# Kernel tuning notes

Hardware: AMD Instinct MI355X
Metric: run time of the kernel (lower is better)

## Reference

```python
import jax, jax.numpy as jnp
import numpy as np

DIM = 512
BATCH, SEQ = 4, 4096


def setup_inputs() -> dict:
    key = jax.random.key(0)
    kx, kq, kk, kv, ko = jax.random.split(key, 5)
    s = DIM ** -0.5  # fan-in style init scale for stability
    return {
        "x": jax.random.normal(kx, (BATCH, SEQ, DIM), dtype=jnp.float32),
        "Wq": jax.random.normal(kq, (DIM, DIM), dtype=jnp.float32) * s,
        "Wk": jax.random.normal(kk, (DIM, DIM), dtype=jnp.float32) * s,
        "Wv": jax.random.normal(kv, (DIM, DIM), dtype=jnp.float32) * s,
        "Wo": jax.random.normal(ko, (DIM, DIM), dtype=jnp.float32) * s,
    }


def reference(x, Wq, Wk, Wv, Wo):
    # x: [B, S, D]; projections (torch Linear, no bias -> x @ W here)
    q = jnp.einsum('bsd,dk->bsk', x, Wq)  # [B,S,K]
    k = jnp.einsum('bsd,dk->bsk', x, Wk)  # [B,S,K]
    v = jnp.einsum('bsd,dv->bsv', x, Wv)  # [B,S,V]

    # sequential recurrence: M_t = M_{t-1} + v_t k_t^T ; y_t = M_t q_t
    def step(M, qkv_t):
        q_t, k_t, v_t = qkv_t  # each [B, K] / [B, V]
        M = M + v_t[:, :, None] * k_t[:, None, :]  # [B, V, K]
        y_t = jnp.einsum('bvk,bk->bv', M, q_t)
        return M, y_t

    M0 = jnp.zeros((x.shape[0], Wv.shape[1], Wk.shape[1]), dtype=x.dtype)
    qT = jnp.swapaxes(q, 0, 1)  # [S,B,K]
    kT = jnp.swapaxes(k, 0, 1)
    vT = jnp.swapaxes(v, 0, 1)
    _, ys = jax.lax.scan(step, M0, (qT, kT, vT))  # ys: [S,B,V]
    y = jnp.swapaxes(ys, 0, 1)  # [B,S,V]
    return jnp.einsum('bsv,vd->bsd', y, Wo)
```

## Files before the change

kernel.cpp:

```cpp
#include <hip/hip_runtime.h>
#include <hip/hip_bf16.h>

typedef __attribute__((ext_vector_type(8))) short bf16x8;
typedef __attribute__((ext_vector_type(4))) float f32x4;

__device__ inline short f2bf(float f) {
    __hip_bfloat16 h = __float2bfloat16(f);
    short s;
    __builtin_memcpy(&s, &h, 2);
    return s;
}
__device__ inline float bf2f(short s) {
    unsigned int u = ((unsigned int)(unsigned short)s) << 16;
    float f;
    __builtin_memcpy(&f, &u, 4);
    return f;
}

__device__ inline void cp16_async(const void* g, void* l) {
    __builtin_amdgcn_global_load_lds(
        (const __attribute__((address_space(1))) void*)g,
        (__attribute__((address_space(3))) void*)l, 16, 0, 0);
}


__global__ void prep_kernel(const float* __restrict__ x, short* __restrict__ Xb,
                            const float* __restrict__ W0, const float* __restrict__ W1,
                            const float* __restrict__ W2, const float* __restrict__ W3,
                            short* __restrict__ W4T) {
    int bid = blockIdx.x;
    if (bid < 8192) {
        int i = bid * 256 + threadIdx.x;
        float4 f = ((const float4*)x)[i];
        union { short s[4]; int2 v; } u;
        u.s[0] = f2bf(f.x); u.s[1] = f2bf(f.y); u.s[2] = f2bf(f.z); u.s[3] = f2bf(f.w);
        ((int2*)Xb)[i] = u.v;
    } else {
        int i = (bid - 8192) * 256 + threadIdx.x;
        int w = i >> 18;
        int r = i & 262143;
        int n = r >> 9, k = r & 511;
        const float* W = (w == 0) ? W0 : (w == 1) ? W1 : (w == 2) ? W2 : W3;
        W4T[i] = f2bf(W[k * 512 + n]);
    }
}


#define LDS_DECL __shared__ short sA0[4096], sA1[4096], sB0[4096], sB1[4096]

__device__ inline void mfma_kloop64(const short* __restrict__ A, int lda,
                                    const short* __restrict__ B, int ldb,
                                    int Kd, f32x4* acc,
                                    short* sA0, short* sA1, short* sB0, short* sB1) {
    const int tid = threadIdx.x, lane = tid & 63, wv = tid >> 6;
    const int quad = lane >> 4, lr = lane & 15;
    const int wr = (wv >> 1) * 64, wc = (wv & 1) * 64;
    const int c0 = tid, c1 = tid + 256;
    const int r0 = c0 >> 2, k80 = (c0 & 3) * 8;
    const int r1 = c1 >> 2, k81 = (c1 & 3) * 8;

    for (int k0 = 0; k0 < Kd; k0 += 64) {
        __syncthreads();
        cp16_async(A + (size_t)r0 * lda + k0 + k80,      sA0 + c0 * 8);
        cp16_async(A + (size_t)r1 * lda + k0 + k81,      sA0 + c1 * 8);
        cp16_async(A + (size_t)r0 * lda + k0 + 32 + k80, sA1 + c0 * 8);
        cp16_async(A + (size_t)r1 * lda + k0 + 32 + k81, sA1 + c1 * 8);
        cp16_async(B + (size_t)r0 * ldb + k0 + k80,      sB0 + c0 * 8);
        cp16_async(B + (size_t)r1 * ldb + k0 + k81,      sB0 + c1 * 8);
        cp16_async(B + (size_t)r0 * ldb + k0 + 32 + k80, sB1 + c0 * 8);
        cp16_async(B + (size_t)r1 * ldb + k0 + 32 + k81, sB1 + c1 * 8);
        __syncthreads();
#pragma unroll
        for (int half = 0; half < 2; ++half) {
            const short* pa = half ? sA1 : sA0;
            const short* pb = half ? sB1 : sB0;
            bf16x8 af[4], bfr[4];
#pragma unroll
            for (int i = 0; i < 4; ++i)
                af[i] = *(const bf16x8*)&pa[(wr + i * 16 + lr) * 32 + quad * 8];
#pragma unroll
            for (int j = 0; j < 4; ++j)
                bfr[j] = *(const bf16x8*)&pb[(wc + j * 16 + lr) * 32 + quad * 8];
#pragma unroll
            for (int i = 0; i < 4; ++i)
#pragma unroll
                for (int j = 0; j < 4; ++j)
                    acc[i * 4 + j] = __builtin_amdgcn_mfma_f32_16x16x32_bf16(af[i], bfr[j], acc[i * 4 + j], 0, 0, 0);
        }
    }
}

__device__ inline void store_out(float* p, float v) { *p = v; }
__device__ inline void store_out(short* p, float v) { *p = f2bf(v); }

template <typename OutT>
__device__ inline void store_tile128(OutT* C, int ldc, const f32x4* acc) {
    const int lane = threadIdx.x & 63, wv = threadIdx.x >> 6;
    const int quad = lane >> 4, lr = lane & 15;
    const int wr = (wv >> 1) * 64, wc = (wv & 1) * 64;
#pragma unroll
    for (int i = 0; i < 4; ++i)
#pragma unroll
        for (int j = 0; j < 4; ++j)
#pragma unroll
            for (int r = 0; r < 4; ++r)
                store_out(&C[(size_t)(wr + i * 16 + quad * 4 + r) * ldc + wc + j * 16 + lr],
                          acc[i * 4 + j][r]);
}

__global__ __launch_bounds__(256, 4) void proj_all(const short* __restrict__ Xb,
                                                   const short* __restrict__ W4T,
                                                   short* __restrict__ Qb, short* __restrict__ Kb,
                                                   short* __restrict__ Vt, short* __restrict__ Kt) {
    LDS_DECL;
    f32x4 acc[16];
#pragma unroll
    for (int i = 0; i < 16; ++i) acc[i] = (f32x4){0.f, 0.f, 0.f, 0.f};
    const int bid = blockIdx.x;
    const int lane = threadIdx.x & 63, wv = threadIdx.x >> 6;
    const int quad = lane >> 4, lr = lane & 15;
    const int wr = (wv >> 1) * 64, wc = (wv & 1) * 64;
    if (bid < 1024) {
        const int mt = bid >> 3, by = bid & 7;
        const short* At = Xb + (size_t)mt * 128 * 512;
        const short* Bt = W4T + (size_t)by * 128 * 512;
        short* Ct = ((by < 4) ? Qb : Kb) + (size_t)mt * 128 * 512 + (by & 3) * 128;
        mfma_kloop64(At, 512, Bt, 512, 512, acc, sA0, sA1, sB0, sB1);
        store_tile128(Ct, 512, acc);
        if (by >= 4) {
            const int b = mt >> 5;
            const int t0b = (mt & 31) * 128;
            const int f0 = (by - 4) * 128;
#pragma unroll
            for (int i = 0; i < 4; ++i)
#pragma unroll
                for (int j = 0; j < 4; ++j) {
                    int f = f0 + wc + j * 16 + lr;
                    int tt0 = t0b + wr + i * 16 + quad * 4;
                    short tmp[4];
#pragma unroll
                    for (int r = 0; r < 4; ++r) tmp[r] = f2bf(acc[i * 4 + j][r]);
                    *(int2*)&Kt[((size_t)b * 512 + f) * 4096 + tt0] = *(const int2*)tmp;
                }
        }
    } else {
        const int r = bid - 1024;
        const int b = r & 3, tt = (r >> 2) & 31, ft = r >> 7;
        const short* At = W4T + (size_t)2 * 262144 + (size_t)ft * 128 * 512;
        const short* Bt = Xb + ((size_t)b * 4096 + tt * 128) * 512;
        short* Ct = Vt + (size_t)b * 512 * 4096 + (size_t)ft * 128 * 4096 + tt * 128;
        mfma_kloop64(At, 512, Bt, 512, 512, acc, sA0, sA1, sB0, sB1);
        store_tile128(Ct, 4096, acc);
    }
}


__global__ __launch_bounds__(256, 4) void phaseA(const short* __restrict__ Vt,
                                                 const short* __restrict__ Kt,
                                                 short* __restrict__ AM) {
    LDS_DECL;
    const int bc = blockIdx.z, b = bc >> 4, c = bc & 15;
    const short* Ap = Vt + ((size_t)b * 512 + blockIdx.x * 128) * 4096 + c * 256;
    const short* Bp = Kt + ((size_t)b * 512 + blockIdx.y * 128) * 4096 + c * 256;
    short* Cp = AM + (size_t)bc * 262144 + (size_t)blockIdx.x * 128 * 512 + blockIdx.y * 128;
    f32x4 acc[16];
#pragma unroll
    for (int i = 0; i < 16; ++i) acc[i] = (f32x4){0.f, 0.f, 0.f, 0.f};
    mfma_kloop64(Ap, 4096, Bp, 4096, 256, acc, sA0, sA1, sB0, sB1);
    store_tile128(Cp, 512, acc);
}

__global__ __launch_bounds__(256, 4) void scan_phaseS(short* __restrict__ AM,
                                                      const short* __restrict__ Q,
                                                      const short* __restrict__ K,
                                                      short* __restrict__ P) {
    LDS_DECL;
    if (blockIdx.x < 512) {
        int i = blockIdx.x * 256 + threadIdx.x;
        int b = i >> 15;
        int vk8 = i & 32767;
        size_t base = (size_t)b * 16 * 262144 + (size_t)vk8 * 8;
        float acc[8];
#pragma unroll
        for (int s = 0; s < 8; ++s) acc[s] = 0.f;
        for (int c = 0; c < 16; ++c) {
            short* p = AM + base + (size_t)c * 262144;
            short in8[8];
            *(int4*)in8 = *(const int4*)p;
            short out8[8];
#pragma unroll
            for (int s = 0; s < 8; ++s) out8[s] = f2bf(acc[s]);
            *(int4*)p = *(const int4*)out8;
#pragma unroll
            for (int s = 0; s < 8; ++s) acc[s] += bf2f(in8[s]);
        }
        return;
    }
    const int e = blockIdx.x - 512;
    const int bc = e >> 2, mt = e & 1, nt = (e >> 1) & 1;
    if (mt < nt) return;
    const int b = bc >> 4, c = bc & 15;
    short* Pt = P + (size_t)bc * 65536 + (size_t)mt * 128 * 256 + nt * 128;
    const short* Ap = Q + ((size_t)(b * 4096 + c * 256 + mt * 128)) * 512;
    const short* Bp = K + ((size_t)(b * 4096 + c * 256 + nt * 128)) * 512;
    f32x4 acc[16];
#pragma unroll
    for (int i = 0; i < 16; ++i) acc[i] = (f32x4){0.f, 0.f, 0.f, 0.f};
    mfma_kloop64(Ap, 512, Bp, 512, 512, acc, sA0, sA1, sB0, sB1);
    const int lane = threadIdx.x & 63, wv = threadIdx.x >> 6;
    const int quad = lane >> 4, lr = lane & 15;
    const int wr = (wv >> 1) * 64, wc = (wv & 1) * 64;
    const bool diag = (mt == nt);
#pragma unroll
    for (int i = 0; i < 4; ++i)
#pragma unroll
        for (int j = 0; j < 4; ++j)
#pragma unroll
            for (int r = 0; r < 4; ++r) {
                int t = wr + i * 16 + quad * 4 + r;
                int jj = wc + j * 16 + lr;
                float v = (!diag || jj <= t) ? acc[i * 4 + j][r] : 0.f;
                Pt[(size_t)t * 256 + jj] = f2bf(v);
            }
}

__global__ __launch_bounds__(256, 4) void phaseY(const short* __restrict__ Q,
                                                 const short* __restrict__ Mpre,
                                                 const short* __restrict__ P,
                                                 const short* __restrict__ Vt,
                                                 short* __restrict__ Y) {
    LDS_DECL;
    const int bc = blockIdx.z, b = bc >> 4, c = bc & 15;
    const int mt = blockIdx.x, nt = blockIdx.y;
    f32x4 acc[16];
#pragma unroll
    for (int i = 0; i < 16; ++i) acc[i] = (f32x4){0.f, 0.f, 0.f, 0.f};
    const short* Ai = Q + ((size_t)(b * 4096 + c * 256 + mt * 128)) * 512;
    const short* Bi = Mpre + (size_t)bc * 262144 + (size_t)nt * 128 * 512;
    mfma_kloop64(Ai, 512, Bi, 512, 512, acc, sA0, sA1, sB0, sB1);
    const short* Ap = P + (size_t)bc * 65536 + (size_t)mt * 128 * 256;
    const short* Bv = Vt + ((size_t)b * 512 + nt * 128) * 4096 + c * 256;
    mfma_kloop64(Ap, 256, Bv, 4096, (mt + 1) * 128, acc, sA0, sA1, sB0, sB1);
    short* Cp = Y + ((size_t)(b * 4096 + c * 256 + mt * 128)) * 512 + nt * 128;
    store_tile128(Cp, 512, acc);
}

template <typename OutT>
__global__ __launch_bounds__(256, 4) void gemm128(const short* __restrict__ A, int lda,
                                                  const short* __restrict__ B, int ldb,
                                                  OutT* __restrict__ C, int ldc, int Kd) {
    LDS_DECL;
    const short* At = A + (size_t)blockIdx.x * 128 * lda;
    const short* Bt = B + (size_t)blockIdx.y * 128 * ldb;
    OutT* Ct = C + (size_t)blockIdx.x * 128 * ldc + blockIdx.y * 128;
    f32x4 acc[16];
#pragma unroll
    for (int i = 0; i < 16; ++i) acc[i] = (f32x4){0.f, 0.f, 0.f, 0.f};
    mfma_kloop64(At, lda, Bt, ldb, Kd, acc, sA0, sA1, sB0, sB1);
    store_tile128(Ct, ldc, acc);
}


extern "C" void kernel_launch(void* const* d_in, const int* in_sizes, int n_in,
                              void* d_out, int out_size, void* d_ws, size_t ws_size,
                              hipStream_t stream) {
    const float* x  = (const float*)d_in[0];
    const float* Wq = (const float*)d_in[1];
    const float* Wk = (const float*)d_in[2];
    const float* Wv = (const float*)d_in[3];
    const float* Wo = (const float*)d_in[4];
    float* out = (float*)d_out;

    const size_t NTD = 16384 * 512;

    short* ws  = (short*)d_ws;
    short* Xb  = ws;
    short* Qb  = Xb + NTD;
    short* Kb  = Qb + NTD;
    short* Kt  = Kb + NTD;
    short* Vt  = Kt + NTD;
    short* P   = Vt + NTD;
    short* W4T = P + 4194304;
    short* AM  = W4T + 1048576;
    short* Yb  = Kb;

    short* WoT = W4T + 3 * 262144;

    prep_kernel<<<12288, 256, 0, stream>>>(x, Xb, Wq, Wk, Wv, Wo, W4T);
    proj_all<<<1536, 256, 0, stream>>>(Xb, W4T, Qb, Kb, Vt, Kt);
    phaseA<<<dim3(4, 4, 64), 256, 0, stream>>>(Vt, Kt, AM);
    scan_phaseS<<<768, 256, 0, stream>>>(AM, Qb, Kb, P);
    phaseY<<<dim3(2, 4, 64), 256, 0, stream>>>(Qb, AM, P, Vt, Yb);
    gemm128<float><<<dim3(128, 4), 256, 0, stream>>>(Yb, 512, WoT, 512, out, 512, 512);
}
```

Baseline: 222.0 us.

## Widen projection and chunk-state GEMM tiles, transpose weights via LDS, flatten grids

Weight transposition in the prep kernel now stages 64x64 tiles through shared memory, so global reads and writes are coalesced instead of strided. The projection and chunk-state (phaseA) GEMMs move to 128x256 tiles with 32 accumulators per thread, which increases operand reuse and halves block counts. All kernels use 1D grids with launch bounds lowered to 2 waves-per-SIMD occupancy, and the output projection becomes a dedicated kernel. The wider tiles double LDS and register use, so fewer blocks fit per CU and latency hiding may suffer.

Measured after the change: 222.1 us. About the same (+0.0%).

```diff
diff --git a/kernel.cpp b/kernel.cpp
--- a/kernel.cpp
+++ b/kernel.cpp
@@ -23,30 +23,44 @@
         (__attribute__((address_space(3))) void*)l, 16, 0, 0);
 }
 
-
 __global__ void prep_kernel(const float* __restrict__ x, short* __restrict__ Xb,
                             const float* __restrict__ W0, const float* __restrict__ W1,
                             const float* __restrict__ W2, const float* __restrict__ W3,
                             short* __restrict__ W4T) {
-    int bid = blockIdx.x;
+    __shared__ short sT[64][72];
+    const int bid = blockIdx.x, tid = threadIdx.x;
     if (bid < 8192) {
-        int i = bid * 256 + threadIdx.x;
+        int i = bid * 256 + tid;
         float4 f = ((const float4*)x)[i];
         union { short s[4]; int2 v; } u;
         u.s[0] = f2bf(f.x); u.s[1] = f2bf(f.y); u.s[2] = f2bf(f.z); u.s[3] = f2bf(f.w);
         ((int2*)Xb)[i] = u.v;
-    } else {
-        int i = (bid - 8192) * 256 + threadIdx.x;
-        int w = i >> 18;
-        int r = i & 262143;
-        int n = r >> 9, k = r & 511;
-        const float* W = (w == 0) ? W0 : (w == 1) ? W1 : (w == 2) ? W2 : W3;
-        W4T[i] = f2bf(W[k * 512 + n]);
-    }
-}
-
-
-#define LDS_DECL __shared__ short sA0[4096], sA1[4096], sB0[4096], sB1[4096]
+        return;
+    }
+    const int wb = bid - 8192;
+    const int w = wb >> 6, r = wb & 63;
+    const int n0 = (r >> 3) * 64, k0 = (r & 7) * 64;
+    const float* W = (w == 0) ? W0 : (w == 1) ? W1 : (w == 2) ? W2 : W3;
+#pragma unroll
+    for (int rr = 0; rr < 4; ++rr) {
+        int c = rr * 256 + tid;
+        int row = c >> 4, col4 = (c & 15) * 4;
+        float4 f = *(const float4*)&W[(size_t)(k0 + row) * 512 + n0 + col4];
+        sT[col4 + 0][row] = f2bf(f.x);
+        sT[col4 + 1][row] = f2bf(f.y);
+        sT[col4 + 2][row] = f2bf(f.z);
+        sT[col4 + 3][row] = f2bf(f.w);
+    }
+    __syncthreads();
+#pragma unroll
+    for (int rr = 0; rr < 2; ++rr) {
+        int c = rr * 256 + tid;
+        int f = c >> 3, k8 = (c & 7) * 8;
+        int4 v = *(const int4*)&sT[f][k8];
+        *(int4*)&W4T[(size_t)w * 262144 + (size_t)(n0 + f) * 512 + k0 + k8] = v;
+    }
+}
+
 
 __device__ inline void mfma_kloop64(const short* __restrict__ A, int lda,
                                     const short* __restrict__ B, int ldb,
@@ -108,75 +122,142 @@
                           acc[i * 4 + j][r]);
 }
 
-__global__ __launch_bounds__(256, 4) void proj_all(const short* __restrict__ Xb,
-                                                   const short* __restrict__ W4T,
-                                                   short* __restrict__ Qb, short* __restrict__ Kb,
-                                                   short* __restrict__ Vt, short* __restrict__ Kt) {
-    LDS_DECL;
-    f32x4 acc[16];
-#pragma unroll
-    for (int i = 0; i < 16; ++i) acc[i] = (f32x4){0.f, 0.f, 0.f, 0.f};
-    const int bid = blockIdx.x;
+
+__device__ inline void mfma_kloop64_wide(const short* __restrict__ A, int lda,
+                                         const short* __restrict__ B, int ldb,
+                                         int Kd, f32x4* acc,
+                                         short* sA0, short* sA1, short* sB0, short* sB1) {
+    const int tid = threadIdx.x, lane = tid & 63, wv = tid >> 6;
+    const int quad = lane >> 4, lr = lane & 15;
+    const int wr = (wv >> 1) * 64, wc = (wv & 1) * 128;
+
+    for (int k0 = 0; k0 < Kd; k0 += 64) {
+        __syncthreads();
+#pragma unroll
+        for (int rr = 0; rr < 2; ++rr) {
+            int c = rr * 256 + tid;
+            int row = c >> 2, k8 = (c & 3) * 8;
+            cp16_async(A + (size_t)row * lda + k0 + k8,      sA0 + c * 8);
+            cp16_async(A + (size_t)row * lda + k0 + 32 + k8, sA1 + c * 8);
+        }
+#pragma unroll
+        for (int rr = 0; rr < 4; ++rr) {
+            int c = rr * 256 + tid;
+            int row = c >> 2, k8 = (c & 3) * 8;
+            cp16_async(B + (size_t)row * ldb + k0 + k8,      sB0 + c * 8);
+            cp16_async(B + (size_t)row * ldb + k0 + 32 + k8, sB1 + c * 8);
+        }
+        __syncthreads();
+#pragma unroll
+        for (int half = 0; half < 2; ++half) {
+            const short* pa = half ? sA1 : sA0;
+            const short* pb = half ? sB1 : sB0;
+            bf16x8 af[4], bfr[8];
+#pragma unroll
+            for (int i = 0; i < 4; ++i)
+                af[i] = *(const bf16x8*)&pa[(wr + i * 16 + lr) * 32 + quad * 8];
+#pragma unroll
+            for (int j = 0; j < 8; ++j)
+                bfr[j] = *(const bf16x8*)&pb[(wc + j * 16 + lr) * 32 + quad * 8];
+#pragma unroll
+            for (int i = 0; i < 4; ++i)
+#pragma unroll
+                for (int j = 0; j < 8; ++j)
+                    acc[i * 8 + j] = __builtin_amdgcn_mfma_f32_16x16x32_bf16(af[i], bfr[j], acc[i * 8 + j], 0, 0, 0);
+        }
+    }
+}
+
+template <typename OutT>
+__device__ inline void store_tile_wide(OutT* C, int ldc, const f32x4* acc) {
     const int lane = threadIdx.x & 63, wv = threadIdx.x >> 6;
     const int quad = lane >> 4, lr = lane & 15;
-    const int wr = (wv >> 1) * 64, wc = (wv & 1) * 64;
-    if (bid < 1024) {
-        const int mt = bid >> 3, by = bid & 7;
+    const int wr = (wv >> 1) * 64, wc = (wv & 1) * 128;
+#pragma unroll
+    for (int i = 0; i < 4; ++i)
+#pragma unroll
+        for (int j = 0; j < 8; ++j)
+#pragma unroll
+            for (int r = 0; r < 4; ++r)
+                store_out(&C[(size_t)(wr + i * 16 + quad * 4 + r) * ldc + wc + j * 16 + lr],
+                          acc[i * 8 + j][r]);
+}
+
+#define LDS_NARROW __shared__ short sA0[4096], sA1[4096], sB0[4096], sB1[4096]
+#define LDS_WIDE   __shared__ short sA0[4096], sA1[4096], sB0[8192], sB1[8192]
+
+__global__ __launch_bounds__(256, 2) void proj_wide(const short* __restrict__ Xb,
+                                                    const short* __restrict__ W4T,
+                                                    short* __restrict__ Qb, short* __restrict__ Kb,
+                                                    short* __restrict__ Vt, short* __restrict__ Kt) {
+    LDS_WIDE;
+    f32x4 acc[32];
+#pragma unroll
+    for (int i = 0; i < 32; ++i) acc[i] = (f32x4){0.f, 0.f, 0.f, 0.f};
+    const int vb = blockIdx.x;
+    const int lane = threadIdx.x & 63, wv = threadIdx.x >> 6;
+    const int quad = lane >> 4, lr = lane & 15;
+    const int wr = (wv >> 1) * 64, wc = (wv & 1) * 128;
+    if (vb < 512) {
+        const int mt = vb >> 2, ny = vb & 3;
+        const int isK = (ny >= 2), nt = ny & 1;
         const short* At = Xb + (size_t)mt * 128 * 512;
-        const short* Bt = W4T + (size_t)by * 128 * 512;
-        short* Ct = ((by < 4) ? Qb : Kb) + (size_t)mt * 128 * 512 + (by & 3) * 128;
-        mfma_kloop64(At, 512, Bt, 512, 512, acc, sA0, sA1, sB0, sB1);
-        store_tile128(Ct, 512, acc);
-        if (by >= 4) {
+        const short* Bt = W4T + ((size_t)isK * 512 + nt * 256) * 512;
+        short* Ct = (isK ? Kb : Qb) + (size_t)mt * 128 * 512 + nt * 256;
+        mfma_kloop64_wide(At, 512, Bt, 512, 512, acc, sA0, sA1, sB0, sB1);
+        store_tile_wide(Ct, 512, acc);
+        if (isK) {
             const int b = mt >> 5;
             const int t0b = (mt & 31) * 128;
-            const int f0 = (by - 4) * 128;
-#pragma unroll
-            for (int i = 0; i < 4; ++i)
-#pragma unroll
-                for (int j = 0; j < 4; ++j) {
+            const int f0 = nt * 256;
+#pragma unroll
+            for (int i = 0; i < 4; ++i)
+#pragma unroll
+                for (int j = 0; j < 8; ++j) {
                     int f = f0 + wc + j * 16 + lr;
                     int tt0 = t0b + wr + i * 16 + quad * 4;
                     short tmp[4];
 #pragma unroll
-                    for (int r = 0; r < 4; ++r) tmp[r] = f2bf(acc[i * 4 + j][r]);
+                    for (int r = 0; r < 4; ++r) tmp[r] = f2bf(acc[i * 8 + j][r]);
                     *(int2*)&Kt[((size_t)b * 512 + f) * 4096 + tt0] = *(const int2*)tmp;
                 }
         }
     } else {
-        const int r = bid - 1024;
-        const int b = r & 3, tt = (r >> 2) & 31, ft = r >> 7;
+        const int g = vb - 512;
+        const int b = g & 3, tt = (g >> 2) & 15, ft = g >> 6;
         const short* At = W4T + (size_t)2 * 262144 + (size_t)ft * 128 * 512;
-        const short* Bt = Xb + ((size_t)b * 4096 + tt * 128) * 512;
-        short* Ct = Vt + (size_t)b * 512 * 4096 + (size_t)ft * 128 * 4096 + tt * 128;
-        mfma_kloop64(At, 512, Bt, 512, 512, acc, sA0, sA1, sB0, sB1);
-        store_tile128(Ct, 4096, acc);
-    }
-}
-
-
-__global__ __launch_bounds__(256, 4) void phaseA(const short* __restrict__ Vt,
-                                                 const short* __restrict__ Kt,
-                                                 short* __restrict__ AM) {
-    LDS_DECL;
-    const int bc = blockIdx.z, b = bc >> 4, c = bc & 15;
-    const short* Ap = Vt + ((size_t)b * 512 + blockIdx.x * 128) * 4096 + c * 256;
-    const short* Bp = Kt + ((size_t)b * 512 + blockIdx.y * 128) * 4096 + c * 256;
-    short* Cp = AM + (size_t)bc * 262144 + (size_t)blockIdx.x * 128 * 512 + blockIdx.y * 128;
-    f32x4 acc[16];
-#pragma unroll
-    for (int i = 0; i < 16; ++i) acc[i] = (f32x4){0.f, 0.f, 0.f, 0.f};
-    mfma_kloop64(Ap, 4096, Bp, 4096, 256, acc, sA0, sA1, sB0, sB1);
-    store_tile128(Cp, 512, acc);
-}
-
-__global__ __launch_bounds__(256, 4) void scan_phaseS(short* __restrict__ AM,
-                                                      const short* __restrict__ Q,
-                                                      const short* __restrict__ K,
-                                                      short* __restrict__ P) {
-    LDS_DECL;
+        const short* Bt = Xb + ((size_t)b * 4096 + tt * 256) * 512;
+        short* Ct = Vt + (size_t)b * 512 * 4096 + (size_t)ft * 128 * 4096 + tt * 256;
+        mfma_kloop64_wide(At, 512, Bt, 512, 512, acc, sA0, sA1, sB0, sB1);
+        store_tile_wide(Ct, 4096, acc);
+    }
+}
+
+__global__ __launch_bounds__(256, 2) void phaseA_wide(const short* __restrict__ Vt,
+                                                      const short* __restrict__ Kt,
+                                                      short* __restrict__ AM) {
+    LDS_WIDE;
+    const int vb = blockIdx.x;
+    const int mt = vb & 3, nt = (vb >> 2) & 1, bc = vb >> 3;
+    const int b = bc >> 4, c = bc & 15;
+    const short* Ap = Vt + ((size_t)b * 512 + mt * 128) * 4096 + c * 256;
+    const short* Bp = Kt + ((size_t)b * 512 + nt * 256) * 4096 + c * 256;
+    short* Cp = AM + (size_t)bc * 262144 + (size_t)mt * 128 * 512 + nt * 256;
+    f32x4 acc[32];
+#pragma unroll
+    for (int i = 0; i < 32; ++i) acc[i] = (f32x4){0.f, 0.f, 0.f, 0.f};
+    mfma_kloop64_wide(Ap, 4096, Bp, 4096, 256, acc, sA0, sA1, sB0, sB1);
+    store_tile_wide(Cp, 512, acc);
+}
+
+__global__ __launch_bounds__(256, 2) void scan_phaseS_k(short* __restrict__ AM,
+                                                        const short* __restrict__ Q,
+                                                        const short* __restrict__ K,
+                                                        short* __restrict__ P) {
+    LDS_NARROW;
+    const int tid = threadIdx.x;
     if (blockIdx.x < 512) {
-        int i = blockIdx.x * 256 + threadIdx.x;
+        int i = blockIdx.x * 256 + tid;
         int b = i >> 15;
         int vk8 = i & 32767;
         size_t base = (size_t)b * 16 * 262144 + (size_t)vk8 * 8;
@@ -207,7 +288,7 @@
 #pragma unroll
     for (int i = 0; i < 16; ++i) acc[i] = (f32x4){0.f, 0.f, 0.f, 0.f};
     mfma_kloop64(Ap, 512, Bp, 512, 512, acc, sA0, sA1, sB0, sB1);
-    const int lane = threadIdx.x & 63, wv = threadIdx.x >> 6;
+    const int lane = tid & 63, wv = tid >> 6;
     const int quad = lane >> 4, lr = lane & 15;
     const int wr = (wv >> 1) * 64, wc = (wv & 1) * 64;
     const bool diag = (mt == nt);
@@ -224,14 +305,15 @@
             }
 }
 
-__global__ __launch_bounds__(256, 4) void phaseY(const short* __restrict__ Q,
-                                                 const short* __restrict__ Mpre,
-                                                 const short* __restrict__ P,
-                                                 const short* __restrict__ Vt,
-                                                 short* __restrict__ Y) {
-    LDS_DECL;
-    const int bc = blockIdx.z, b = bc >> 4, c = bc & 15;
-    const int mt = blockIdx.x, nt = blockIdx.y;
+__global__ __launch_bounds__(256, 2) void phaseY_k(const short* __restrict__ Q,
+                                                   const short* __restrict__ Mpre,
+                                                   const short* __restrict__ P,
+                                                   const short* __restrict__ Vt,
+                                                   short* __restrict__ Y) {
+    LDS_NARROW;
+    const int vb = blockIdx.x;
+    const int mt = vb & 1, nt = (vb >> 1) & 3, bc = vb >> 3;
+    const int b = bc >> 4, c = bc & 15;
     f32x4 acc[16];
 #pragma unroll
     for (int i = 0; i < 16; ++i) acc[i] = (f32x4){0.f, 0.f, 0.f, 0.f};
@@ -245,19 +327,19 @@
     store_tile128(Cp, 512, acc);
 }
 
-template <typename OutT>
-__global__ __launch_bounds__(256, 4) void gemm128(const short* __restrict__ A, int lda,
-                                                  const short* __restrict__ B, int ldb,
-                                                  OutT* __restrict__ C, int ldc, int Kd) {
-    LDS_DECL;
-    const short* At = A + (size_t)blockIdx.x * 128 * lda;
-    const short* Bt = B + (size_t)blockIdx.y * 128 * ldb;
-    OutT* Ct = C + (size_t)blockIdx.x * 128 * ldc + blockIdx.y * 128;
+__global__ __launch_bounds__(256, 2) void outproj_k(const short* __restrict__ Y,
+                                                    const short* __restrict__ W4T,
+                                                    float* __restrict__ out) {
+    LDS_NARROW;
+    const int mt = blockIdx.x >> 2, nt = blockIdx.x & 3;
+    const short* At = Y + (size_t)mt * 128 * 512;
+    const short* Bt = W4T + (size_t)3 * 262144 + (size_t)nt * 128 * 512;
+    float* Ct = out + (size_t)mt * 128 * 512 + nt * 128;
     f32x4 acc[16];
 #pragma unroll
     for (int i = 0; i < 16; ++i) acc[i] = (f32x4){0.f, 0.f, 0.f, 0.f};
-    mfma_kloop64(At, lda, Bt, ldb, Kd, acc, sA0, sA1, sB0, sB1);
-    store_tile128(Ct, ldc, acc);
+    mfma_kloop64(At, 512, Bt, 512, 512, acc, sA0, sA1, sB0, sB1);
+    store_tile128(Ct, 512, acc);
 }
 
 
@@ -284,12 +366,10 @@
     short* AM  = W4T + 1048576;
     short* Yb  = Kb;
 
-    short* WoT = W4T + 3 * 262144;
-
-    prep_kernel<<<12288, 256, 0, stream>>>(x, Xb, Wq, Wk, Wv, Wo, W4T);
-    proj_all<<<1536, 256, 0, stream>>>(Xb, W4T, Qb, Kb, Vt, Kt);
-    phaseA<<<dim3(4, 4, 64), 256, 0, stream>>>(Vt, Kt, AM);
-    scan_phaseS<<<768, 256, 0, stream>>>(AM, Qb, Kb, P);
-    phaseY<<<dim3(2, 4, 64), 256, 0, stream>>>(Qb, AM, P, Vt, Yb);
-    gemm128<float><<<dim3(128, 4), 256, 0, stream>>>(Yb, 512, WoT, 512, out, 512, 512);
-}
+    prep_kernel<<<8448, 256, 0, stream>>>(x, Xb, Wq, Wk, Wv, Wo, W4T);
+    proj_wide<<<768, 256, 0, stream>>>(Xb, W4T, Qb, Kb, Vt, Kt);
+    phaseA_wide<<<512, 256, 0, stream>>>(Vt, Kt, AM);
+    scan_phaseS_k<<<768, 256, 0, stream>>>(AM, Qb, Kb, P);
+    phaseY_k<<<512, 256, 0, stream>>>(Qb, AM, P, Vt, Yb);
+    outproj_k<<<512, 256, 0, stream>>>(Yb, W4T, out);
+}
```
